# Kernel optimization log

Hardware: AMD Instinct MI355X
Metric: run time of the kernel (lower is better)

The kernel has to match this reference:

```python
import jax, jax.numpy as jnp
import numpy as np

EPS = 1e-5

def conv2d(x, w, b=None, pad=0):
    y = jax.lax.conv_general_dilated(x, w, (1, 1), [(pad, pad), (pad, pad)],
                                     dimension_numbers=('NCHW', 'OIHW', 'NCHW'))
    if b is not None:
        y = y + b[None, :, None, None]
    return y

def bn(x, w, b, m, v):
    scale = w / jnp.sqrt(v + EPS)
    return x * scale[None, :, None, None] + (b - m * scale)[None, :, None, None]

def setup_inputs() -> dict:
    key = jax.random.key(0)
    ks = jax.random.split(key, 24)
    B, Cin, H, W = 4, 2048, 60, 60
    Ci = Cin // 4           # inter_channels = 512
    Cq = Ci // 8            # q/k dim = 64
    Cout = 59
    r = lambda k, s, sc=0.05: jax.random.normal(k, s, jnp.float32) * sc
    return {
        'x': jax.random.normal(ks[0], (B, Cin, H, W), jnp.float32),
        'dep': jax.random.uniform(ks[1], (B, 1, H, W), jnp.float32),
        'w5a': r(ks[2], (Ci, Cin, 3, 3)),
        'bn1_w': jax.random.uniform(ks[3], (Ci,), jnp.float32, 0.5, 1.5),
        'bn1_b': r(ks[4], (Ci,)),
        'bn1_m': r(ks[5], (Ci,)),
        'bn1_v': jax.random.uniform(ks[6], (Ci,), jnp.float32, 0.5, 1.5),
        'wq': r(ks[7], (Cq, Ci, 1, 1)), 'bq': r(ks[8], (Cq,)),
        'wk': r(ks[9], (Cq, Ci, 1, 1)), 'bk': r(ks[10], (Cq,)),
        'wv': r(ks[11], (Ci, Ci, 1, 1)), 'bv': r(ks[12], (Ci,)),
        'gamma': r(ks[13], (1,), 0.5),
        'lamb1': r(ks[14], (1,), 0.5),
        'w51': r(ks[15], (Ci, Ci, 3, 3)),
        'bn2_w': jax.random.uniform(ks[16], (Ci,), jnp.float32, 0.5, 1.5),
        'bn2_b': r(ks[17], (Ci,)),
        'bn2_m': r(ks[18], (Ci,)),
        'bn2_v': jax.random.uniform(ks[19], (Ci,), jnp.float32, 0.5, 1.5),
        'w6': r(ks[20], (Cout, Ci, 1, 1)), 'b6': r(ks[21], (Cout,)),
    }

def reference(x, dep, w5a, bn1_w, bn1_b, bn1_m, bn1_v, wq, bq, wk, bk, wv, bv,
              gamma, lamb1, w51, bn2_w, bn2_b, bn2_m, bn2_v, w6, b6):
    # conv5a: 3x3 conv -> BN (inference) -> ReLU
    f1 = jax.nn.relu(bn(conv2d(x, w5a, pad=1), bn1_w, bn1_b, bn1_m, bn1_v))
    B, C, H, W = f1.shape
    N = H * W
    q = conv2d(f1, wq, bq).reshape(B, -1, N)     # [B, C/8, N]
    k = conv2d(f1, wk, bk).reshape(B, -1, N)     # [B, C/8, N]
    v = conv2d(f1, wv, bv).reshape(B, C, N)      # [B, C, N]
    energy = jnp.einsum('bci,bcj->bij', q, k)    # [B, N, N]
    d1 = dep.reshape(B, 1, N)
    d = jnp.transpose(d1, (0, 2, 1)) - d1        # [B, N, N] depth difference
    sim = energy - lamb1[0] * jnp.square(d)      # dep_order == 2
    attn = jax.nn.softmax(sim, axis=-1)
    # out[b,c,i] = sum_j v[b,c,j] * attn[b,i,j]  (bmm with attn^T)
    out = jnp.einsum('bcj,bij->bci', v, attn).reshape(B, C, H, W)
    sa = gamma[0] * out + f1
    sc = jax.nn.relu(bn(conv2d(sa, w51, pad=1), bn2_w, bn2_b, bn2_m, bn2_v))
    # Dropout2d in eval mode is identity
    logits = conv2d(sc, w6, b6)
    return (logits,)
```

## Files before the change

### kernel.cpp

```cpp
#include <hip/hip_runtime.h>
#include <math.h>

typedef unsigned short u16;
typedef short s16x8 __attribute__((ext_vector_type(8)));
typedef float f32x4 __attribute__((ext_vector_type(4)));

#define HW 3600
#define WID 60
#define SIMS 3616
#define AROWS 3712
#define SP 4216
#define PCIN 2048

__device__ __forceinline__ u16 f2bf(float f){
  unsigned u = __float_as_uint(f);
  unsigned r = (u + 0x7fffu + ((u>>16)&1u)) >> 16;
  return (u16)r;
}
__device__ __forceinline__ float bf2f(u16 b){ return __uint_as_float(((unsigned)b)<<16); }

__device__ __forceinline__ void gl2lds16(const void* g, void* l){
  __builtin_amdgcn_global_load_lds((const __attribute__((address_space(1))) unsigned*)g,
                                   (__attribute__((address_space(3))) unsigned*)l, 16, 0, 0);
}

__device__ __forceinline__ float4 ldg4(const float* __restrict__ p){
  return *reinterpret_cast<const float4*>(p);
}
__device__ __forceinline__ float waveMax(float v){
  #pragma unroll
  for(int o=32;o>0;o>>=1) v = fmaxf(v, __shfl_xor(v,o,64));
  return v;
}
__device__ __forceinline__ float waveSum(float v){
  #pragma unroll
  for(int o=32;o>0;o>>=1) v += __shfl_xor(v,o,64);
  return v;
}

__global__ void bn_prep(const float* __restrict__ w1, const float* __restrict__ b1,
                        const float* __restrict__ m1, const float* __restrict__ v1,
                        const float* __restrict__ w2, const float* __restrict__ b2,
                        const float* __restrict__ m2, const float* __restrict__ v2,
                        float* __restrict__ sc1, float* __restrict__ sh1,
                        float* __restrict__ sc2, float* __restrict__ sh2){
  int i = threadIdx.x;
  if(i < 512){
    float s1 = w1[i] / sqrtf(v1[i] + 1e-5f);
    sc1[i] = s1; sh1[i] = b1[i] - m1[i]*s1;
    float s2 = w2[i] / sqrtf(v2[i] + 1e-5f);
    sc2[i] = s2; sh2[i] = b2[i] - m2[i]*s2;
  }
}

__global__ __launch_bounds__(256) void pack_x(const float* __restrict__ x, u16* __restrict__ xpadT){
  __shared__ float tile[64][65];
  const int b = blockIdx.z, sp0 = blockIdx.x*64, ci0 = blockIdx.y*64;
  const int t = threadIdx.x, tc = t & 63, tr = t >> 6;
  const float* xb = x + ((size_t)b*PCIN + ci0)*HW;
  #pragma unroll
  for(int l=0;l<16;l++){
    int ci = tr + l*4;
    int sp = sp0 + tc;
    float v = 0.f;
    if(sp < SP){
      int j = sp / 68, c = sp - j*68;
      int jj = j-1, cc = c-1;
      if((unsigned)jj < 60u && (unsigned)cc < 60u) v = xb[(size_t)ci*HW + jj*60 + cc];
    }
    tile[ci][tc] = v;
  }
  __syncthreads();
  const size_t PL = (size_t)4*SP*PCIN;
  u16* outb = xpadT + (size_t)b*SP*PCIN;
  #pragma unroll
  for(int l=0;l<16;l++){
    int spr = tr + l*4;
    int sp = sp0 + spr;
    if(sp < SP){
      float v = tile[tc][spr];
      u16 hh = f2bf(v);
      u16 ll = f2bf(v - bf2f(hh));
      size_t o = (size_t)sp*PCIN + ci0 + tc;
      outb[o] = hh;
      outb[o + PL] = ll;
    }
  }
}

__global__ __launch_bounds__(256) void pack_w5a(const float* __restrict__ w, u16* __restrict__ out){
  const int ci = blockIdx.x*256 + threadIdx.x;
  const int m  = blockIdx.y;
  const int rs = blockIdx.z;
  float v = w[((size_t)m*PCIN + ci)*9 + rs];
  u16 hh = f2bf(v);
  u16 ll = f2bf(v - bf2f(hh));
  size_t base = ((size_t)rs*512 + m)*6144;
  out[base + ci]        = hh;
  out[base + 2048 + ci] = ll;
  out[base + 4096 + ci] = hh;
}

__global__ __launch_bounds__(256) void pack_w51(const float* __restrict__ w, u16* __restrict__ out){
  const int ci = blockIdx.x*256 + threadIdx.x;
  const int m  = blockIdx.y;
  const int rs = blockIdx.z;
  float v = w[((size_t)m*512 + ci)*9 + rs];
  out[((size_t)rs*512 + m)*512 + ci] = f2bf(v);
}

template<int MODE>
__global__ __launch_bounds__(256) void mfma_gemm(
    const u16* __restrict__ A, const u16* __restrict__ B,
    const float* __restrict__ scale, const float* __restrict__ shift,
    const float* __restrict__ f1, const float* __restrict__ gamma,
    float* __restrict__ outF, u16* __restrict__ outH)
{
  constexpr int CIC = (MODE==0)? 2048 : 512;
  constexpr int KRS = (MODE==0)? 6144 : 512;
  constexpr int KPR = KRS/32;
  constexpr int NSTEP = (MODE==2)? (SIMS/32) : (9*KPR);

  __shared__ __align__(16) u16 lds[8192];

  const int t  = threadIdx.x;
  const int b  = blockIdx.z;
  const int m0 = blockIdx.x << 7;
  const int nb = blockIdx.y;

  const int sm = t & 127;
  const int kc = t >> 7;

  const u16* Abase;
  if constexpr(MODE==2) Abase = A + (size_t)b*512*SIMS + (size_t)(m0+sm)*SIMS + kc*8;
  else                  Abase = A + (size_t)(m0+sm)*KRS + kc*8;

  const u16* Bb = nullptr; int spb = 0;
  if constexpr(MODE==2){
    Bb = B + (size_t)b*AROWS*SIMS + (size_t)(nb*128 + sm)*SIMS + kc*8;
  } else {
    int seg = sm >> 6, wl = sm & 63;
    spb = (nb*2 + seg)*68 + wl;
    Bb = B + (size_t)b*SP*CIC + kc*8;
  }

  u16* ldsA0 = &lds[(size_t)t*8];
  u16* ldsA1 = &lds[(size_t)t*8 + 2048];
  u16* ldsB0 = &lds[4096 + (size_t)t*8];
  u16* ldsB1 = &lds[4096 + (size_t)t*8 + 2048];

  f32x4 acc[4][4];
  #pragma unroll
  for(int i=0;i<4;i++)
    #pragma unroll
    for(int j=0;j<4;j++) acc[i][j] = (f32x4){0.f,0.f,0.f,0.f};

  const int lane = t & 63;
  const int wv = t >> 6;
  const int wm = (wv>>1)<<6, wn = (wv&1)<<6;
  const int fr = lane & 15, fq = lane >> 4;
  const char* ldsc = (const char*)lds;
  const int aoff = fq*2048 + (wm+fr)*16;
  const int boff = 8192 + fq*2048 + (wn+fr)*16;

  for(int st=0; st<NSTEP; ++st){
    int rs, k0;
    if constexpr(MODE==2){ rs = 0; k0 = st<<5; }
    else { rs = st/KPR; k0 = (st - rs*KPR)<<5; }

    __syncthreads();
    const u16* ga;
    if constexpr(MODE==2) ga = Abase + k0;
    else                  ga = Abase + (size_t)rs*512*KRS + k0;
    gl2lds16(ga,      ldsA0);
    gl2lds16(ga + 16, ldsA1);
    const u16* gb;
    if constexpr(MODE==2){ gb = Bb + k0; }
    else {
      int r = rs/3, s = rs - r*3;
      int plane = (MODE==0) ? (k0>>12) : 0;
      int ci0 = k0 & (CIC-1);
      gb = Bb + (size_t)plane*((size_t)4*SP*PCIN) + (size_t)(spb + r*68 + s)*CIC + ci0;
    }
    gl2lds16(gb,      ldsB0);
    gl2lds16(gb + 16, ldsB1);
    __syncthreads();

    s16x8 af[4], bg[4];
    #pragma unroll
    for(int i=0;i<4;i++) af[i] = *(const s16x8*)(ldsc + aoff + i*256);
    #pragma unroll
    for(int j=0;j<4;j++) bg[j] = *(const s16x8*)(ldsc + boff + j*256);
    #pragma unroll
    for(int i=0;i<4;i++)
      #pragma unroll
      for(int j=0;j<4;j++)
        acc[i][j] = __builtin_amdgcn_mfma_f32_16x16x32_bf16(af[i], bg[j], acc[i][j], 0,0,0);
  }

  if constexpr(MODE==0 || MODE==1){
    #pragma unroll
    for(int i=0;i<4;i++){
      #pragma unroll
      for(int q=0;q<4;q++){
        int m = m0 + wm + i*16 + fq*4 + q;
        float scl = scale[m], shf = shift[m];
        #pragma unroll
        for(int j=0;j<4;j++){
          int np = nb*128 + wn + j*16 + fr;
          int h = np>>6, w = np&63;
          if(w < 60){
            float v = fmaxf(fmaf(acc[i][j][q], scl, shf), 0.f);
            size_t o = ((size_t)b*512 + m)*HW + h*60 + w;
            if constexpr(MODE==0) outF[o] = v;
            else                  outH[o] = f2bf(v);
          }
        }
      }
    }
  } else {
    float g = gamma[0];
    #pragma unroll
    for(int j=0;j<4;j++){
      int ip = nb*128 + wn + j*16 + fr;
      if(ip < HW){
        int h = ip/60, w = ip - h*60;
        size_t spo = (size_t)b*SP*512 + (size_t)((h+1)*68 + (w+1))*512;
        #pragma unroll
        for(int i=0;i<4;i++){
          #pragma unroll
          for(int q=0;q<4;q++){
            int m = m0 + wm + i*16 + fq*4 + q;
            float v = fmaf(g, acc[i][j][q], f1[((size_t)b*512 + m)*HW + ip]);
            outH[spo + m] = f2bf(v);
          }
        }
      }
    }
  }
}

template<bool INBF, bool GM, bool OUTBF>
__global__ __launch_bounds__(256) void gemm1x1(const void* __restrict__ inv,
    const float* __restrict__ w, const float* __restrict__ bias,
    float* __restrict__ outF, u16* __restrict__ outH, int M, int K, int OS)
{
  const int b  = blockIdx.z;
  const int m0 = blockIdx.x * 64;
  const int n0 = blockIdx.y * 64;
  const int t  = threadIdx.x;
  const int tm = t >> 4, tn = t & 15;

  __shared__ __align__(16) float As[16][64];
  __shared__ __align__(16) float Bs[16][64];

  float acc[4][4] = {};

  const int arow = t >> 2, acol = (t & 3) << 2;
  const int bkk  = t & 15, bnl  = (t >> 4) << 2;
  const bool bvalid = (n0 + bnl) < HW;

  for(int k0 = 0; k0 < K; k0 += 16){
    float4 av = make_float4(0.f,0.f,0.f,0.f);
    if(!GM || (m0 + arow) < M)
      av = ldg4(&w[(size_t)(m0 + arow)*K + k0 + acol]);
    As[acol+0][arow] = av.x;
    As[acol+1][arow] = av.y;
    As[acol+2][arow] = av.z;
    As[acol+3][arow] = av.w;

    float4 bv = make_float4(0.f,0.f,0.f,0.f);
    if(bvalid){
      if constexpr(INBF){
        const u16* inb = (const u16*)inv + (size_t)b*K*HW;
        const u16* p = &inb[(size_t)(k0 + bkk)*HW + n0 + bnl];
        bv.x = bf2f(p[0]); bv.y = bf2f(p[1]); bv.z = bf2f(p[2]); bv.w = bf2f(p[3]);
      } else {
        const float* inb = (const float*)inv + (size_t)b*K*HW;
        bv = ldg4(&inb[(size_t)(k0 + bkk)*HW + n0 + bnl]);
      }
    }
    *reinterpret_cast<float4*>(&Bs[bkk][bnl]) = bv;

    __syncthreads();
    #pragma unroll
    for(int kk=0;kk<16;kk++){
      float4 a  = *reinterpret_cast<const float4*>(&As[kk][tm<<2]);
      float4 bb = *reinterpret_cast<const float4*>(&Bs[kk][tn<<2]);
      float ar[4] = {a.x,a.y,a.z,a.w};
      float br[4] = {bb.x,bb.y,bb.z,bb.w};
      #pragma unroll
      for(int ii=0;ii<4;ii++)
        #pragma unroll
        for(int jj=0;jj<4;jj++)
          acc[ii][jj] = fmaf(ar[ii], br[jj], acc[ii][jj]);
    }
    __syncthreads();
  }

  int n = n0 + (tn<<2);
  if(n < OS){
    #pragma unroll
    for(int ii=0;ii<4;ii++){
      int m = m0 + (tm<<2) + ii;
      if(!GM || m < M){
        float bi = bias[m];
        #pragma unroll
        for(int jj=0;jj<4;jj++){
          int nn = n + jj;
          float val = (nn < HW) ? (acc[ii][jj] + bi) : 0.f;
          if constexpr(OUTBF) outH[((size_t)b*M + m)*OS + nn] = f2bf(val);
          else                outF[((size_t)b*M + m)*OS + nn] = val;
        }
      }
    }
  }
}

__global__ __launch_bounds__(256) void energy_sim(
    const float* __restrict__ q, const float* __restrict__ kptr,
    const float* __restrict__ dep, const float* __restrict__ lamb1,
    float* __restrict__ sim)
{
  const int i0 = blockIdx.y * 64;
  const int j0 = blockIdx.x * 64;
  const int t  = threadIdx.x;
  const int tm = t >> 4, tn = t & 15;

  __shared__ __align__(16) float Qs[64][64];
  __shared__ __align__(16) float Ks[64][64];

  {
    const int cc = t >> 4;
    const int il = (t & 15) << 2;
    #pragma unroll
    for(int it=0; it<4; it++){
      int c = cc + it*16;
      float4 qv = make_float4(0.f,0.f,0.f,0.f);
      float4 kv = make_float4(0.f,0.f,0.f,0.f);
      if(i0 + il < HW) qv = ldg4(&q[(size_t)c*HW + i0 + il]);
      if(j0 + il < HW) kv = ldg4(&kptr[(size_t)c*HW + j0 + il]);
      *reinterpret_cast<float4*>(&Qs[c][il]) = qv;
      *reinterpret_cast<float4*>(&Ks[c][il]) = kv;
    }
  }
  __syncthreads();

  float acc[4][4] = {};
  #pragma unroll 4
  for(int c=0;c<64;c++){
    float4 a  = *reinterpret_cast<const float4*>(&Qs[c][tm<<2]);
    float4 bv = *reinterpret_cast<const float4*>(&Ks[c][tn<<2]);
    float ar[4] = {a.x,a.y,a.z,a.w};
    float br[4] = {bv.x,bv.y,bv.z,bv.w};
    #pragma unroll
    for(int ii=0;ii<4;ii++)
      #pragma unroll
      for(int jj=0;jj<4;jj++)
        acc[ii][jj] = fmaf(ar[ii], br[jj], acc[ii][jj]);
  }

  float lam = lamb1[0];
  float di[4], dj[4];
  #pragma unroll
  for(int ii=0;ii<4;ii++){ int i = i0+(tm<<2)+ii; di[ii] = (i<HW)? dep[i] : 0.f; }
  #pragma unroll
  for(int jj=0;jj<4;jj++){ int j = j0+(tn<<2)+jj; dj[jj] = (j<HW)? dep[j] : 0.f; }

  int j = j0 + (tn<<2);
  if(j < HW){
    #pragma unroll
    for(int ii=0;ii<4;ii++){
      int i = i0 + (tm<<2) + ii;
      if(i < HW){
        float4 o;
        float d0 = di[ii]-dj[0]; o.x = acc[ii][0] - lam*d0*d0;
        float d1 = di[ii]-dj[1]; o.y = acc[ii][1] - lam*d1*d1;
        float d2 = di[ii]-dj[2]; o.z = acc[ii][2] - lam*d2*d2;
        float d3 = di[ii]-dj[3]; o.w = acc[ii][3] - lam*d3*d3;
        *reinterpret_cast<float4*>(&sim[(size_t)i*SIMS + j]) = o;
      }
    }
  }
}

__global__ __launch_bounds__(256) void softmax_attn(float* __restrict__ sim, u16* __restrict__ attn){
  __shared__ float red[8];
  const int row = blockIdx.x;
  float* p = sim + (size_t)row*SIMS;
  u16*   a = attn + (size_t)row*SIMS;
  const int wid = threadIdx.x >> 6, lane = threadIdx.x & 63;

  float m = -3.4e38f;
  for(int j=threadIdx.x; j<HW; j+=256) m = fmaxf(m, p[j]);
  m = waveMax(m);
  if(lane==0) red[wid] = m;
  __syncthreads();
  if(threadIdx.x==0) red[4] = fmaxf(fmaxf(red[0],red[1]), fmaxf(red[2],red[3]));
  __syncthreads();
  m = red[4];

  float s = 0.f;
  for(int j=threadIdx.x; j<HW; j+=256){ float e = expf(p[j]-m); p[j] = e; s += e; }
  s = waveSum(s);
  if(lane==0) red[wid] = s;
  __syncthreads();
  if(threadIdx.x==0) red[5] = red[0]+red[1]+red[2]+red[3];
  __syncthreads();
  float inv = 1.0f / red[5];
  for(int j=threadIdx.x; j<HW; j+=256) a[j] = f2bf(p[j] * inv);
  if(threadIdx.x < SIMS-HW) a[HW + threadIdx.x] = 0;
}

extern "C" void kernel_launch(void* const* d_in, const int* in_sizes, int n_in,
                              void* d_out, int out_size, void* d_ws, size_t ws_size,
                              hipStream_t stream)
{
  const float* x    = (const float*)d_in[0];
  const float* dep  = (const float*)d_in[1];
  const float* w5a  = (const float*)d_in[2];
  const float* bn1w = (const float*)d_in[3];
  const float* bn1b = (const float*)d_in[4];
  const float* bn1m = (const float*)d_in[5];
  const float* bn1v = (const float*)d_in[6];
  const float* wq   = (const float*)d_in[7];
  const float* bq   = (const float*)d_in[8];
  const float* wk   = (const float*)d_in[9];
  const float* bk   = (const float*)d_in[10];
  const float* wv   = (const float*)d_in[11];
  const float* bv   = (const float*)d_in[12];
  const float* gamma= (const float*)d_in[13];
  const float* lamb1= (const float*)d_in[14];
  const float* w51  = (const float*)d_in[15];
  const float* bn2w = (const float*)d_in[16];
  const float* bn2b = (const float*)d_in[17];
  const float* bn2m = (const float*)d_in[18];
  const float* bn2v = (const float*)d_in[19];
  const float* w6   = (const float*)d_in[20];
  const float* b6   = (const float*)d_in[21];
  float* out = (float*)d_out;

  char* cur = (char*)d_ws;
  auto alloc = [&](size_t bytes)->char*{ char* p = cur; cur += (bytes + 255) & ~(size_t)255; return p; };

  float* sc1 = (float*)alloc(512*4);
  float* sh1 = (float*)alloc(512*4);
  float* sc2 = (float*)alloc(512*4);
  float* sh2 = (float*)alloc(512*4);
  u16* xpadT = (u16*)alloc((size_t)2*4*SP*PCIN*2);
  u16* W5ab  = (u16*)alloc((size_t)9*512*6144*2);
  u16* W51b  = (u16*)alloc((size_t)9*512*512*2);
  float* f1  = (float*)alloc((size_t)4*512*HW*4);
  float* qb  = (float*)alloc((size_t)4*64*HW*4);
  float* kb  = (float*)alloc((size_t)4*64*HW*4);
  u16* vb    = (u16*)alloc((size_t)4*512*SIMS*2);
  float* sim = (float*)alloc((size_t)HW*SIMS*4);
  u16* attn  = (u16*)alloc((size_t)4*AROWS*SIMS*2);
  u16* sapadT= (u16*)alloc((size_t)4*SP*512*2);
  u16* scb   = (u16*)alloc((size_t)4*512*HW*2);

  bn_prep<<<1, 512, 0, stream>>>(bn1w,bn1b,bn1m,bn1v, bn2w,bn2b,bn2m,bn2v,
                                 sc1,sh1,sc2,sh2);

  hipMemsetAsync(sapadT, 0, (size_t)4*SP*512*2, stream);

  pack_x  <<<dim3(66,32,4), 256, 0, stream>>>(x, xpadT);
  pack_w5a<<<dim3(8,512,9), 256, 0, stream>>>(w5a, W5ab);
  pack_w51<<<dim3(2,512,9), 256, 0, stream>>>(w51, W51b);

  mfma_gemm<0><<<dim3(4,30,4), 256, 0, stream>>>(W5ab, xpadT, sc1, sh1,
                                                 nullptr, nullptr, f1, nullptr);

  gemm1x1<false,false,false><<<dim3(1,57,4), 256, 0, stream>>>(f1, wq, bq, qb, nullptr, 64, 512, HW);
  gemm1x1<false,false,false><<<dim3(1,57,4), 256, 0, stream>>>(f1, wk, bk, kb, nullptr, 64, 512, HW);
  gemm1x1<false,false,true ><<<dim3(8,57,4), 256, 0, stream>>>(f1, wv, bv, nullptr, vb, 512, 512, SIMS);

  for(int b=0;b<4;b++){
    energy_sim<<<dim3(57,57), 256, 0, stream>>>(qb + (size_t)b*64*HW,
                                                kb + (size_t)b*64*HW,
                                                dep + (size_t)b*HW, lamb1, sim);
    softmax_attn<<<HW, 256, 0, stream>>>(sim, attn + (size_t)b*AROWS*SIMS);
  }

  mfma_gemm<2><<<dim3(4,29,4), 256, 0, stream>>>(vb, attn, nullptr, nullptr,
                                                 f1, gamma, nullptr, sapadT);

  mfma_gemm<1><<<dim3(4,30,4), 256, 0, stream>>>(W51b, sapadT, sc2, sh2,
                                                 nullptr, nullptr, nullptr, scb);

  gemm1x1<true,true,false><<<dim3(1,57,4), 256, 0, stream>>>(scb, w6, b6, out, nullptr, 59, 512, HW);
}
```

Measured before the change: 3.169 ms.

## Triple-buffer MFMA GEMM with 512 threads, XCD-aware tile swizzle, online softmax

```diff
diff --git a/kernel.cpp b/kernel.cpp
--- a/kernel.cpp
+++ b/kernel.cpp
@@ -26,16 +26,6 @@
 
 __device__ __forceinline__ float4 ldg4(const float* __restrict__ p){
   return *reinterpret_cast<const float4*>(p);
-}
-__device__ __forceinline__ float waveMax(float v){
-  #pragma unroll
-  for(int o=32;o>0;o>>=1) v = fmaxf(v, __shfl_xor(v,o,64));
-  return v;
-}
-__device__ __forceinline__ float waveSum(float v){
-  #pragma unroll
-  for(int o=32;o>0;o>>=1) v += __shfl_xor(v,o,64);
-  return v;
 }
 
 __global__ void bn_prep(const float* __restrict__ w1, const float* __restrict__ b1,
@@ -110,7 +100,7 @@
 }
 
 template<int MODE>
-__global__ __launch_bounds__(256) void mfma_gemm(
+__global__ __launch_bounds__(512) void mfma_gemm(
     const u16* __restrict__ A, const u16* __restrict__ B,
     const float* __restrict__ scale, const float* __restrict__ shift,
     const float* __restrict__ f1, const float* __restrict__ gamma,
@@ -120,83 +110,113 @@
   constexpr int KRS = (MODE==0)? 6144 : 512;
   constexpr int KPR = KRS/32;
   constexpr int NSTEP = (MODE==2)? (SIMS/32) : (9*KPR);
-
-  __shared__ __align__(16) u16 lds[8192];
+  constexpr int NTA = (MODE==2)? 116 : 120;
+  constexpr int NB  = (MODE==2)? 29  : 30;
+
+  __shared__ __align__(16) u16 lds[3*8192];
 
   const int t  = threadIdx.x;
-  const int b  = blockIdx.z;
-  const int m0 = blockIdx.x << 7;
-  const int nb = blockIdx.y;
-
-  const int sm = t & 127;
-  const int kc = t >> 7;
+
+  const int wg = blockIdx.x;
+  const int chunk = (4*NTA) >> 3;
+  const int wgid = (wg & 7) * chunk + (wg >> 3);
+  const int mt = wgid / NTA;
+  const int nt = wgid - mt*NTA;
+  const int m0 = mt << 7;
+  const int b  = nt / NB;
+  const int nb = nt - b*NB;
+
+  const int srow = t & 127;
+  const int skc  = t >> 7;
 
   const u16* Abase;
-  if constexpr(MODE==2) Abase = A + (size_t)b*512*SIMS + (size_t)(m0+sm)*SIMS + kc*8;
-  else                  Abase = A + (size_t)(m0+sm)*KRS + kc*8;
-
-  const u16* Bb = nullptr; int spb = 0;
+  if constexpr(MODE==2) Abase = A + (size_t)b*512*SIMS + (size_t)(m0+srow)*SIMS + skc*8;
+  else                  Abase = A + (size_t)(m0+srow)*KRS + skc*8;
+
+  const u16* Bbase;
   if constexpr(MODE==2){
-    Bb = B + (size_t)b*AROWS*SIMS + (size_t)(nb*128 + sm)*SIMS + kc*8;
+    Bbase = B + (size_t)b*AROWS*SIMS + (size_t)(nb*128 + srow)*SIMS + skc*8;
   } else {
-    int seg = sm >> 6, wl = sm & 63;
-    spb = (nb*2 + seg)*68 + wl;
-    Bb = B + (size_t)b*SP*CIC + kc*8;
-  }
-
-  u16* ldsA0 = &lds[(size_t)t*8];
-  u16* ldsA1 = &lds[(size_t)t*8 + 2048];
-  u16* ldsB0 = &lds[4096 + (size_t)t*8];
-  u16* ldsB1 = &lds[4096 + (size_t)t*8 + 2048];
-
-  f32x4 acc[4][4];
+    int seg = srow >> 6, wl = srow & 63;
+    int spb = (nb*2 + seg)*68 + wl;
+    Bbase = B + (size_t)b*SP*CIC + (size_t)spb*CIC + skc*8;
+  }
+  const size_t PL = (size_t)4*SP*PCIN;
+
+  f32x4 acc[4][2];
   #pragma unroll
   for(int i=0;i<4;i++)
     #pragma unroll
-    for(int j=0;j<4;j++) acc[i][j] = (f32x4){0.f,0.f,0.f,0.f};
+    for(int j=0;j<2;j++) acc[i][j] = (f32x4){0.f,0.f,0.f,0.f};
 
   const int lane = t & 63;
   const int wv = t >> 6;
-  const int wm = (wv>>1)<<6, wn = (wv&1)<<6;
+  const int wm = (wv >> 2) << 6;
+  const int wn = (wv & 3) << 5;
   const int fr = lane & 15, fq = lane >> 4;
   const char* ldsc = (const char*)lds;
   const int aoff = fq*2048 + (wm+fr)*16;
   const int boff = 8192 + fq*2048 + (wn+fr)*16;
 
-  for(int st=0; st<NSTEP; ++st){
-    int rs, k0;
-    if constexpr(MODE==2){ rs = 0; k0 = st<<5; }
-    else { rs = st/KPR; k0 = (st - rs*KPR)<<5; }
-
-    __syncthreads();
+  auto stage = [&](int st, int q){
+    int rs = 0, k0;
+    if constexpr(MODE==2){ k0 = st << 5; }
+    else { rs = st / KPR; k0 = (st - rs*KPR) << 5; }
     const u16* ga;
     if constexpr(MODE==2) ga = Abase + k0;
     else                  ga = Abase + (size_t)rs*512*KRS + k0;
-    gl2lds16(ga,      ldsA0);
-    gl2lds16(ga + 16, ldsA1);
+    gl2lds16(ga, &lds[(size_t)q*8192 + t*8]);
     const u16* gb;
-    if constexpr(MODE==2){ gb = Bb + k0; }
+    if constexpr(MODE==2){ gb = Bbase + k0; }
     else {
       int r = rs/3, s = rs - r*3;
-      int plane = (MODE==0) ? (k0>>12) : 0;
+      int plane = (MODE==0)? (k0 >> 12) : 0;
       int ci0 = k0 & (CIC-1);
-      gb = Bb + (size_t)plane*((size_t)4*SP*PCIN) + (size_t)(spb + r*68 + s)*CIC + ci0;
-    }
-    gl2lds16(gb,      ldsB0);
-    gl2lds16(gb + 16, ldsB1);
-    __syncthreads();
-
-    s16x8 af[4], bg[4];
-    #pragma unroll
-    for(int i=0;i<4;i++) af[i] = *(const s16x8*)(ldsc + aoff + i*256);
-    #pragma unroll
-    for(int j=0;j<4;j++) bg[j] = *(const s16x8*)(ldsc + boff + j*256);
+      gb = Bbase + (size_t)plane*PL + (size_t)(r*68 + s)*CIC + ci0;
+    }
+    gl2lds16(gb, &lds[(size_t)q*8192 + 4096 + t*8]);
+  };
+
+  auto compute = [&](int q){
+    const char* base = ldsc + q*16384;
+    s16x8 af[4], bg[2];
+    #pragma unroll
+    for(int i=0;i<4;i++) af[i] = *(const s16x8*)(base + aoff + i*256);
+    #pragma unroll
+    for(int j=0;j<2;j++) bg[j] = *(const s16x8*)(base + boff + j*256);
+    __builtin_amdgcn_s_setprio(1);
     #pragma unroll
     for(int i=0;i<4;i++)
       #pragma unroll
-      for(int j=0;j<4;j++)
+      for(int j=0;j<2;j++)
         acc[i][j] = __builtin_amdgcn_mfma_f32_16x16x32_bf16(af[i], bg[j], acc[i][j], 0,0,0);
-  }
+    __builtin_amdgcn_s_setprio(0);
+  };
+
+  stage(0, 0);
+  stage(1, 1);
+  int cur = 0;
+  for(int st = 0; st < NSTEP-2; ++st){
+    int q2 = cur + 2; if(q2 >= 3) q2 -= 3;
+    stage(st+2, q2);
+    asm volatile("s_waitcnt vmcnt(4)" ::: "memory");
+    __builtin_amdgcn_s_barrier();
+    asm volatile("" ::: "memory");
+    compute(cur);
+    asm volatile("" ::: "memory");
+    __builtin_amdgcn_s_barrier();
+    asm volatile("" ::: "memory");
+    cur = (cur+1 == 3)? 0 : cur+1;
+  }
+  asm volatile("s_waitcnt vmcnt(2)" ::: "memory");
+  __builtin_amdgcn_s_barrier();
+  asm volatile("" ::: "memory");
+  compute(cur);
+  cur = (cur+1 == 3)? 0 : cur+1;
+  asm volatile("s_waitcnt vmcnt(0)" ::: "memory");
+  __builtin_amdgcn_s_barrier();
+  asm volatile("" ::: "memory");
+  compute(cur);
 
   if constexpr(MODE==0 || MODE==1){
     #pragma unroll
@@ -206,7 +226,7 @@
         int m = m0 + wm + i*16 + fq*4 + q;
         float scl = scale[m], shf = shift[m];
         #pragma unroll
-        for(int j=0;j<4;j++){
+        for(int j=0;j<2;j++){
           int np = nb*128 + wn + j*16 + fr;
           int h = np>>6, w = np&63;
           if(w < 60){
@@ -221,7 +241,7 @@
   } else {
     float g = gamma[0];
     #pragma unroll
-    for(int j=0;j<4;j++){
+    for(int j=0;j<2;j++){
       int ip = nb*128 + wn + j*16 + fr;
       if(ip < HW){
         int h = ip/60, w = ip - h*60;
@@ -384,31 +404,36 @@
   }
 }
 
-__global__ __launch_bounds__(256) void softmax_attn(float* __restrict__ sim, u16* __restrict__ attn){
-  __shared__ float red[8];
+__global__ __launch_bounds__(256) void softmax_attn(const float* __restrict__ sim,
+                                                    u16* __restrict__ attn){
+  __shared__ float redM[4], redS[4];
   const int row = blockIdx.x;
-  float* p = sim + (size_t)row*SIMS;
+  const float* p = sim + (size_t)row*SIMS;
   u16*   a = attn + (size_t)row*SIMS;
   const int wid = threadIdx.x >> 6, lane = threadIdx.x & 63;
 
-  float m = -3.4e38f;
-  for(int j=threadIdx.x; j<HW; j+=256) m = fmaxf(m, p[j]);
-  m = waveMax(m);
-  if(lane==0) red[wid] = m;
+  float m = -3.4e38f, s = 0.f;
+  for(int j=threadIdx.x; j<HW; j+=256){
+    float v = p[j];
+    float mo = m;
+    m = fmaxf(m, v);
+    s = s*__expf(mo - m) + __expf(v - m);
+  }
+  #pragma unroll
+  for(int o=32;o>0;o>>=1){
+    float m2 = __shfl_xor(m, o, 64);
+    float s2 = __shfl_xor(s, o, 64);
+    float mn = fmaxf(m, m2);
+    s = s*__expf(m - mn) + s2*__expf(m2 - mn);
+    m = mn;
+  }
+  if(lane==0){ redM[wid] = m; redS[wid] = s; }
   __syncthreads();
-  if(threadIdx.x==0) red[4] = fmaxf(fmaxf(red[0],red[1]), fmaxf(red[2],red[3]));
-  __syncthreads();
-  m = red[4];
-
-  float s = 0.f;
-  for(int j=threadIdx.x; j<HW; j+=256){ float e = expf(p[j]-m); p[j] = e; s += e; }
-  s = waveSum(s);
-  if(lane==0) red[wid] = s;
-  __syncthreads();
-  if(threadIdx.x==0) red[5] = red[0]+red[1]+red[2]+red[3];
-  __syncthreads();
-  float inv = 1.0f / red[5];
-  for(int j=threadIdx.x; j<HW; j+=256) a[j] = f2bf(p[j] * inv);
+  float M = fmaxf(fmaxf(redM[0],redM[1]), fmaxf(redM[2],redM[3]));
+  float S = redS[0]*__expf(redM[0]-M) + redS[1]*__expf(redM[1]-M)
+          + redS[2]*__expf(redM[2]-M) + redS[3]*__expf(redM[3]-M);
+  float inv = 1.0f / S;
+  for(int j=threadIdx.x; j<HW; j+=256) a[j] = f2bf(__expf(p[j]-M) * inv);
   if(threadIdx.x < SIMS-HW) a[HW + threadIdx.x] = 0;
 }
 
@@ -468,8 +493,8 @@
   pack_w5a<<<dim3(8,512,9), 256, 0, stream>>>(w5a, W5ab);
   pack_w51<<<dim3(2,512,9), 256, 0, stream>>>(w51, W51b);
 
-  mfma_gemm<0><<<dim3(4,30,4), 256, 0, stream>>>(W5ab, xpadT, sc1, sh1,
-                                                 nullptr, nullptr, f1, nullptr);
+  mfma_gemm<0><<<480, 512, 0, stream>>>(W5ab, xpadT, sc1, sh1,
+                                        nullptr, nullptr, f1, nullptr);
 
   gemm1x1<false,false,false><<<dim3(1,57,4), 256, 0, stream>>>(f1, wq, bq, qb, nullptr, 64, 512, HW);
   gemm1x1<false,false,false><<<dim3(1,57,4), 256, 0, stream>>>(f1, wk, bk, kb, nullptr, 64, 512, HW);
@@ -482,11 +507,11 @@
     softmax_attn<<<HW, 256, 0, stream>>>(sim, attn + (size_t)b*AROWS*SIMS);
   }
 
-  mfma_gemm<2><<<dim3(4,29,4), 256, 0, stream>>>(vb, attn, nullptr, nullptr,
-                                                 f1, gamma, nullptr, sapadT);
-
-  mfma_gemm<1><<<dim3(4,30,4), 256, 0, stream>>>(W51b, sapadT, sc2, sh2,
-                                                 nullptr, nullptr, nullptr, scb);
+  mfma_gemm<2><<<464, 512, 0, stream>>>(vb, attn, nullptr, nullptr,
+                                        f1, gamma, nullptr, sapadT);
+
+  mfma_gemm<1><<<480, 512, 0, stream>>>(W51b, sapadT, sc2, sh2,
+                                        nullptr, nullptr, nullptr, scb);
 
   gemm1x1<true,true,false><<<dim3(1,57,4), 256, 0, stream>>>(scb, w6, b6, out, nullptr, 59, 512, HW);
 }
```

Result: slower. 3.242 ms (+2.3%).
